# Kernel optimization log

Hardware: AMD Instinct MI355X
Metric: run time of the kernel (lower is better)

Reference implementation:

```python
import jax, jax.numpy as jnp
import numpy as np

N = 4096; D0 = 1024; D1 = 1280; H0 = 819; H1 = 1024; S = 819; K = 5


def setup_inputs() -> dict:
    key = jax.random.key(0)
    ks = jax.random.split(key, 20)
    def rn(k, shape, scale=1.0):
        return jax.random.normal(k, shape, dtype=jnp.float32) * scale
    inp = {}
    inp['x0'] = rn(ks[0], (N, D0))
    inp['x1'] = rn(ks[1], (N, D1))
    inp['we'] = jax.random.uniform(ks[2], (N, 2), dtype=jnp.float32, minval=0.1, maxval=1.0)
    # scale graphs ~1/100 so row-aggregated features stay in tanh's linear-ish range
    inp['g0'] = rn(ks[3], (N, N), 0.01)
    inp['g1'] = rn(ks[4], (N, N), 0.01)
    # Linear weights stored [in, out] (torch Linear applies x @ W.T + b); xavier-ish scale
    inp['We1_0'] = rn(ks[5], (D0, H0), D0 ** -0.5); inp['be1_0'] = jnp.zeros((H0,), jnp.float32)
    inp['We2_0'] = rn(ks[6], (H0, S), H0 ** -0.5);  inp['be2_0'] = jnp.zeros((S,), jnp.float32)
    inp['We1_1'] = rn(ks[7], (D1, H1), D1 ** -0.5); inp['be1_1'] = jnp.zeros((H1,), jnp.float32)
    inp['We2_1'] = rn(ks[8], (H1, S), H1 ** -0.5);  inp['be2_1'] = jnp.zeros((S,), jnp.float32)
    inp['Wd1_0'] = rn(ks[9], (S, H0), S ** -0.5);   inp['bd1_0'] = jnp.zeros((H0,), jnp.float32)
    inp['Wd2_0'] = rn(ks[10], (H0, D0), H0 ** -0.5); inp['bd2_0'] = jnp.zeros((D0,), jnp.float32)
    inp['Wd1_1'] = rn(ks[11], (S, H1), S ** -0.5);  inp['bd1_1'] = jnp.zeros((H1,), jnp.float32)
    inp['Wd2_1'] = rn(ks[12], (H1, D1), H1 ** -0.5); inp['bd2_1'] = jnp.zeros((D1,), jnp.float32)
    inp['Ww_0'] = rn(ks[13], (S, S), S ** -0.5)
    inp['Ww_1'] = rn(ks[14], (S, S), S ** -0.5)
    inp['Wf_0'] = rn(ks[15], (S, S), S ** -0.5)
    inp['Wf_1'] = rn(ks[16], (S, S), S ** -0.5)
    # stands in for the sklearn spectral-clustering centers (constant w.r.t. autodiff)
    inp['cluster_layer'] = rn(ks[17], (K, S), 0.1)
    return inp


def _gconv2(g, x, W1, b1, W2, b2):
    # tanh(Linear(g @ x)) twice: fusable gather-MLP chain
    h1 = jnp.tanh((g @ x) @ W1 + b1)
    return jnp.tanh((g @ h1) @ W2 + b2)


def reference(x0, x1, we, g0, g1,
              We1_0, be1_0, We2_0, be2_0, We1_1, be1_1, We2_1, be2_1,
              Wd1_0, bd1_0, Wd2_0, bd2_0, Wd1_1, bd1_1, Wd2_1, bd2_1,
              Ww_0, Ww_1, Wf_0, Wf_1, cluster_layer):
    # encoders
    h2_0 = _gconv2(g0, x0, We1_0, be1_0, We2_0, be2_0)  # [N, S]
    h2_1 = _gconv2(g1, x1, We1_1, be1_1, We2_1, be2_1)  # [N, S]
    # diag(we[:,i]) @ h_i  ==  broadcast row-scale (avoids O(N^2) diag matmul)
    weighted_sum = we[:, 0:1] * h2_0 + we[:, 1:2] * h2_1
    z = weighted_sum / jnp.sum(we, axis=1, keepdims=True)  # diag(1/sum) @ ws
    # inner-product adjacency decoders
    adj0 = jax.nn.sigmoid((z @ Ww_0) @ z.T)  # [N, N]
    adj1 = jax.nn.sigmoid((z @ Ww_1) @ z.T)
    # feature decoders with fusion weights
    rec0 = _gconv2(g0, jnp.tanh(z @ Wf_0), Wd1_0, bd1_0, Wd2_0, bd2_0)  # [N, D0]
    rec1 = _gconv2(g1, jnp.tanh(z @ Wf_1), Wd1_1, bd1_1, Wd2_1, bd2_1)  # [N, D1]
    # Student-t soft assignment to cluster centers
    d2 = jnp.sum((z[:, None, :] - cluster_layer[None, :, :]) ** 2, axis=2)  # [N, K]
    q = 1.0 / (1.0 + d2)
    q = q / jnp.sum(q, axis=1, keepdims=True)
    # target distribution p
    w = q ** 2 / jnp.sum(q, axis=0)
    p = w / jnp.sum(w, axis=1, keepdims=True)
    return (rec0, rec1, adj0, adj1, z, p, q, cluster_layer)
```

## Files before the change

### kernel.cpp

```cpp
#include <hip/hip_runtime.h>
#include <hip/hip_bf16.h>
#include <cstdint>
#include <cstddef>

typedef __bf16 bf16;
typedef __attribute__((ext_vector_type(8))) __bf16 bf16x8;
typedef __attribute__((ext_vector_type(4))) __bf16 bf16x4;
typedef __attribute__((ext_vector_type(4))) float f32x4;

__device__ __forceinline__ void gload_lds16(const void* g, void* l) {
  __builtin_amdgcn_global_load_lds(
      (const __attribute__((address_space(1))) uint32_t*)(uintptr_t)g,
      (__attribute__((address_space(3))) uint32_t*)(uintptr_t)l, 16, 0, 0);
}

struct GProb {
  const bf16* A; const bf16* Bt; const float* bias;
  float* Cf; bf16* Cb;
  int K, Npad, ldcf, ldcb, Ntrue, act;
};
struct GBatch { GProb p[4]; };

__global__ __launch_bounds__(256, 2)
void gemm_nt_batch(GBatch b)
{
  const GProb P = b.p[blockIdx.z];
  const long bn = (long)blockIdx.x * 128;
  if (bn >= P.Npad) return;

  __shared__ __align__(16) bf16 As[128 * 32];
  __shared__ __align__(16) bf16 Bs[128 * 32];

  const int K    = P.K;
  const int tid  = threadIdx.x;
  const int lane = tid & 63, wave = tid >> 6;
  const int wr = wave >> 1, wc = wave & 1;
  const int l15 = lane & 15, quad = lane >> 4;
  const long bm = (long)blockIdx.y * 128;

  long aoff[2], boff[2];
  int ldsoff[2];
#pragma unroll
  for (int s = 0; s < 2; ++s) {
    int slot = s * 256 + tid;
    int row = slot >> 2, cs = slot & 3;
    int gc = cs ^ (row & 3);
    aoff[s] = (bm + row) * (long)K + gc * 8;
    boff[s] = (bn + row) * (long)K + gc * 8;
    ldsoff[s] = (s * 256 + wave * 64) * 8;
  }

  const int cfr = (quad ^ (lane & 3)) * 8;
  int afr[4], bfr[4];
#pragma unroll
  for (int i = 0; i < 4; ++i) {
    afr[i] = (wr * 64 + i * 16 + l15) * 32 + cfr;
    bfr[i] = (wc * 64 + i * 16 + l15) * 32 + cfr;
  }

  f32x4 acc[4][4];
#pragma unroll
  for (int i = 0; i < 4; ++i)
#pragma unroll
    for (int j = 0; j < 4; ++j) acc[i][j] = {0.f, 0.f, 0.f, 0.f};

  for (int k0 = 0; k0 < K; k0 += 32) {
    __syncthreads();
    gload_lds16(P.A + aoff[0] + k0, As + ldsoff[0]);
    gload_lds16(P.A + aoff[1] + k0, As + ldsoff[1]);
    gload_lds16(P.Bt + boff[0] + k0, Bs + ldsoff[0]);
    gload_lds16(P.Bt + boff[1] + k0, Bs + ldsoff[1]);
    __syncthreads();

    bf16x8 av[4], bv[4];
#pragma unroll
    for (int i = 0; i < 4; ++i) av[i] = *(const bf16x8*)(As + afr[i]);
#pragma unroll
    for (int j = 0; j < 4; ++j) bv[j] = *(const bf16x8*)(Bs + bfr[j]);
#pragma unroll
    for (int i = 0; i < 4; ++i)
#pragma unroll
      for (int j = 0; j < 4; ++j)
        acc[i][j] = __builtin_amdgcn_mfma_f32_16x16x32_bf16(av[i], bv[j], acc[i][j], 0, 0, 0);
  }

  const long row0 = bm + wr * 64 + quad * 4;
  const long col0 = bn + wc * 64 + l15;
  const int act = P.act;
#pragma unroll
  for (int i = 0; i < 4; ++i) {
#pragma unroll
    for (int j = 0; j < 4; ++j) {
      long c = col0 + j * 16;
      float bb = P.bias ? P.bias[c] : 0.f;
#pragma unroll
      for (int t = 0; t < 4; ++t) {
        long r = row0 + i * 16 + t;
        float v = acc[i][j][t] + bb;
        if (act == 1) v = tanhf(v);
        else if (act == 2) v = 1.f / (1.f + __expf(-v));
        if (P.Cf && c < P.Ntrue) P.Cf[r * P.ldcf + c] = v;
        if (P.Cb) P.Cb[r * P.ldcb + c] = (bf16)v;
      }
    }
  }
}

struct TrBatch {
  const void* src[14]; bf16* dst[14];
  int R[14], C[14], Q[14], nbx[14], isb[14];
  int blkStart[15];
  int nprob;
};

__global__ void tr_batch(TrBatch a)
{
  __shared__ float tile[32][33];
  int pi = 0, b = blockIdx.x;
  while (b >= a.blkStart[pi + 1]) ++pi;
  const int rel = b - a.blkStart[pi];
  const int nbx = a.nbx[pi];
  const int q0 = (rel % nbx) * 32;
  const int p0 = (rel / nbx) * 32;
  const int R = a.R[pi], C = a.C[pi], Q = a.Q[pi];
  const bool isb = a.isb[pi] != 0;
  const void* src = a.src[pi];
  const int tx = threadIdx.x & 31, ty = threadIdx.x >> 5;
#pragma unroll
  for (int y = ty; y < 32; y += 8) {
    int r = q0 + y, c = p0 + tx;
    float v = 0.f;
    if (r < R && c < C)
      v = isb ? (float)((const bf16*)src)[(long)r * C + c]
              : ((const float*)src)[(long)r * C + c];
    tile[y][tx] = v;
  }
  __syncthreads();
  bf16* dst = a.dst[pi];
#pragma unroll
  for (int y = ty; y < 32; y += 8)
    dst[(long)(p0 + y) * Q + (q0 + tx)] = (bf16)tile[tx][y];
}

struct CvtB { const float* s[2]; bf16* d[2]; };
__global__ void cvt_batch(CvtB cb, long n)
{
  const float* s = cb.s[blockIdx.z];
  bf16* d = cb.d[blockIdx.z];
  long i = ((long)blockIdx.x * blockDim.x + threadIdx.x) * 4;
  if (i >= n) return;
  float4 v = *(const float4*)(s + i);
  bf16x4 o = {(bf16)v.x, (bf16)v.y, (bf16)v.z, (bf16)v.w};
  *(bf16x4*)(d + i) = o;
}

__global__ void zkern(const float* __restrict__ h20, const float* __restrict__ h21,
                      const float* __restrict__ we, float* __restrict__ zout,
                      bf16* __restrict__ zb)
{
  const int n = blockIdx.x;
  const float w0 = we[n * 2], w1 = we[n * 2 + 1];
  const float inv = 1.f / (w0 + w1);
  for (int c = threadIdx.x; c < 896; c += 256) {
    float v = (w0 * h20[(long)n * 896 + c] + w1 * h21[(long)n * 896 + c]) * inv;
    zb[(long)n * 896 + c] = (bf16)v;
    if (c < 819) zout[(long)n * 819 + c] = v;
  }
}

__global__ void qkern(const float* __restrict__ z, const float* __restrict__ cl,
                      float* __restrict__ qout)
{
  const int n = blockIdx.x;
  const int lane = threadIdx.x;
  float d0 = 0, d1 = 0, d2 = 0, d3 = 0, d4 = 0;
  for (int s = lane; s < 819; s += 64) {
    float zv = z[(long)n * 819 + s];
    float t0 = zv - cl[0 * 819 + s]; d0 += t0 * t0;
    float t1 = zv - cl[1 * 819 + s]; d1 += t1 * t1;
    float t2 = zv - cl[2 * 819 + s]; d2 += t2 * t2;
    float t3 = zv - cl[3 * 819 + s]; d3 += t3 * t3;
    float t4 = zv - cl[4 * 819 + s]; d4 += t4 * t4;
  }
#pragma unroll
  for (int off = 32; off > 0; off >>= 1) {
    d0 += __shfl_xor(d0, off);
    d1 += __shfl_xor(d1, off);
    d2 += __shfl_xor(d2, off);
    d3 += __shfl_xor(d3, off);
    d4 += __shfl_xor(d4, off);
  }
  if (lane == 0) {
    float q0 = 1.f / (1.f + d0), q1 = 1.f / (1.f + d1), q2 = 1.f / (1.f + d2);
    float q3 = 1.f / (1.f + d3), q4 = 1.f / (1.f + d4);
    float inv = 1.f / (q0 + q1 + q2 + q3 + q4);
    float* qr = qout + (long)n * 5;
    qr[0] = q0 * inv; qr[1] = q1 * inv; qr[2] = q2 * inv;
    qr[3] = q3 * inv; qr[4] = q4 * inv;
  }
}

__global__ void colsum_kern(const float* __restrict__ q, float* __restrict__ colsum)
{
  __shared__ float red[256];
  const int k = blockIdx.x;
  float s = 0.f;
  for (int n = threadIdx.x; n < 4096; n += 256) s += q[(long)n * 5 + k];
  red[threadIdx.x] = s;
  __syncthreads();
  for (int w = 128; w > 0; w >>= 1) {
    if (threadIdx.x < w) red[threadIdx.x] += red[threadIdx.x + w];
    __syncthreads();
  }
  if (threadIdx.x == 0) colsum[k] = red[0];
}

__global__ void pkern(const float* __restrict__ q, const float* __restrict__ colsum,
                      float* __restrict__ p)
{
  int n = blockIdx.x * blockDim.x + threadIdx.x;
  if (n >= 4096) return;
  float w[5], s = 0.f;
#pragma unroll
  for (int k = 0; k < 5; ++k) {
    float qv = q[(long)n * 5 + k];
    w[k] = qv * qv / colsum[k];
    s += w[k];
  }
  float inv = 1.f / s;
#pragma unroll
  for (int k = 0; k < 5; ++k) p[(long)n * 5 + k] = w[k] * inv;
}

struct BiasArgs {
  const float* src[8];
  float* dst[8];
  int n[8];
  int np[8];
};

__global__ void biaspad(BiasArgs a)
{
  int b = blockIdx.x;
  for (int i = threadIdx.x; i < a.np[b]; i += blockDim.x)
    a.dst[b][i] = (i < a.n[b]) ? a.src[b][i] : 0.f;
}

extern "C" void kernel_launch(void* const* d_in, const int* in_sizes, int n_in,
                              void* d_out, int out_size, void* d_ws, size_t ws_size,
                              hipStream_t stream)
{
  (void)in_sizes; (void)n_in; (void)out_size; (void)ws_size;
  const float* x0    = (const float*)d_in[0];
  const float* x1    = (const float*)d_in[1];
  const float* we    = (const float*)d_in[2];
  const float* g0    = (const float*)d_in[3];
  const float* g1    = (const float*)d_in[4];
  const float* We1_0 = (const float*)d_in[5];
  const float* be1_0 = (const float*)d_in[6];
  const float* We2_0 = (const float*)d_in[7];
  const float* be2_0 = (const float*)d_in[8];
  const float* We1_1 = (const float*)d_in[9];
  const float* be1_1 = (const float*)d_in[10];
  const float* We2_1 = (const float*)d_in[11];
  const float* be2_1 = (const float*)d_in[12];
  const float* Wd1_0 = (const float*)d_in[13];
  const float* bd1_0 = (const float*)d_in[14];
  const float* Wd2_0 = (const float*)d_in[15];
  const float* bd2_0 = (const float*)d_in[16];
  const float* Wd1_1 = (const float*)d_in[17];
  const float* bd1_1 = (const float*)d_in[18];
  const float* Wd2_1 = (const float*)d_in[19];
  const float* bd2_1 = (const float*)d_in[20];
  const float* Ww0   = (const float*)d_in[21];
  const float* Ww1   = (const float*)d_in[22];
  const float* Wf0   = (const float*)d_in[23];
  const float* Wf1   = (const float*)d_in[24];
  const float* clus  = (const float*)d_in[25];
  float* out = (float*)d_out;

  const size_t OFF_REC0 = 0;
  const size_t OFF_REC1 = 4194304;
  const size_t OFF_ADJ0 = 9437184;
  const size_t OFF_ADJ1 = 26214400;
  const size_t OFF_Z    = 42991616;
  const size_t OFF_P    = 46346240;
  const size_t OFF_Q    = 46366720;
  const size_t OFF_CL   = 46387200;

  char* ws = (char*)d_ws;
  size_t off = 0;
  auto alloc = [&](size_t bytes) -> void* {
    off = (off + 255) & ~(size_t)255;
    void* p = ws + off;
    off += bytes;
    return p;
  };
  const long N = 4096;
  bf16* g0b   = (bf16*)alloc((size_t)N * 4096 * 2);
  bf16* g1b   = (bf16*)alloc((size_t)N * 4096 * 2);
  bf16* BTe10 = (bf16*)alloc((size_t)896 * 1024 * 2);
  bf16* BTe20 = (bf16*)alloc((size_t)896 * 896 * 2);
  bf16* BTe11 = (bf16*)alloc((size_t)1024 * 1280 * 2);
  bf16* BTe21 = (bf16*)alloc((size_t)896 * 1024 * 2);
  bf16* BTd10 = (bf16*)alloc((size_t)896 * 896 * 2);
  bf16* BTd20 = (bf16*)alloc((size_t)1024 * 896 * 2);
  bf16* BTd11 = (bf16*)alloc((size_t)1024 * 896 * 2);
  bf16* BTd21 = (bf16*)alloc((size_t)1280 * 1024 * 2);
  bf16* BTw0  = (bf16*)alloc((size_t)896 * 896 * 2);
  bf16* BTw1  = (bf16*)alloc((size_t)896 * 896 * 2);
  bf16* BTf0  = (bf16*)alloc((size_t)896 * 896 * 2);
  bf16* BTf1  = (bf16*)alloc((size_t)896 * 896 * 2);
  float* pbe10 = (float*)alloc(896 * 4);
  float* pbe20 = (float*)alloc(896 * 4);
  float* pbe11 = (float*)alloc(1024 * 4);
  float* pbe21 = (float*)alloc(896 * 4);
  float* pbd10 = (float*)alloc(896 * 4);
  float* pbd20 = (float*)alloc(1024 * 4);
  float* pbd11 = (float*)alloc(1024 * 4);
  float* pbd21 = (float*)alloc(1280 * 4);
  float* h20f  = (float*)alloc((size_t)N * 896 * 4);
  float* h21f  = (float*)alloc((size_t)N * 896 * 4);
  bf16* zb     = (bf16*)alloc((size_t)N * 896 * 2);
  float* colsum = (float*)alloc(64);
  bf16* xT0 = (bf16*)alloc((size_t)1024 * 4096 * 2);
  bf16* xT1 = (bf16*)alloc((size_t)1280 * 4096 * 2);
  bf16* u0  = (bf16*)alloc((size_t)N * 1024 * 2);
  bf16* u1  = (bf16*)alloc((size_t)N * 1280 * 2);
  bf16* h0  = (bf16*)alloc((size_t)N * 896 * 2);
  bf16* h1b = (bf16*)alloc((size_t)N * 1024 * 2);
  bf16* y0  = (bf16*)alloc((size_t)N * 896 * 2);
  bf16* y1  = (bf16*)alloc((size_t)N * 896 * 2);
  bf16* t0b = (bf16*)alloc((size_t)N * 896 * 2);
  bf16* t1b = (bf16*)alloc((size_t)N * 896 * 2);

  {
    CvtB cb;
    cb.s[0] = g0; cb.d[0] = g0b;
    cb.s[1] = g1; cb.d[1] = g1b;
    cvt_batch<<<dim3(16384, 1, 2), 256, 0, stream>>>(cb, N * 4096);
  }

  {
    TrBatch tb{};
    tb.nprob = 0; tb.blkStart[0] = 0;
    auto addTr = [&](const void* s, bf16* d, int R, int C, int P, int Q, int isb) {
      int i = tb.nprob++;
      tb.src[i] = s; tb.dst[i] = d;
      tb.R[i] = R; tb.C[i] = C; tb.Q[i] = Q; tb.isb[i] = isb;
      tb.nbx[i] = Q / 32;
      tb.blkStart[i + 1] = tb.blkStart[i] + (Q / 32) * (P / 32);
    };
    addTr(x0, xT0, 4096, 1024, 1024, 4096, 0);
    addTr(x1, xT1, 4096, 1280, 1280, 4096, 0);
    addTr(We1_0, BTe10, 1024, 819, 896, 1024, 0);
    addTr(We2_0, BTe20, 819, 819, 896, 896, 0);
    addTr(We1_1, BTe11, 1280, 1024, 1024, 1280, 0);
    addTr(We2_1, BTe21, 1024, 819, 896, 1024, 0);
    addTr(Wd1_0, BTd10, 819, 819, 896, 896, 0);
    addTr(Wd2_0, BTd20, 819, 1024, 1024, 896, 0);
    addTr(Wd1_1, BTd11, 819, 1024, 1024, 896, 0);
    addTr(Wd2_1, BTd21, 1024, 1280, 1280, 1024, 0);
    addTr(Ww0, BTw0, 819, 819, 896, 896, 0);
    addTr(Ww1, BTw1, 819, 819, 896, 896, 0);
    addTr(Wf0, BTf0, 819, 819, 896, 896, 0);
    addTr(Wf1, BTf1, 819, 819, 896, 896, 0);
    tr_batch<<<tb.blkStart[tb.nprob], 256, 0, stream>>>(tb);
  }

  BiasArgs ba;
  {
    const float* bsrc[8] = {be1_0, be2_0, be1_1, be2_1, bd1_0, bd2_0, bd1_1, bd2_1};
    float* bdst[8] = {pbe10, pbe20, pbe11, pbe21, pbd10, pbd20, pbd11, pbd21};
    int bn_[8] = {819, 819, 1024, 819, 819, 1024, 1024, 1280};
    int bnp[8] = {896, 896, 1024, 896, 896, 1024, 1024, 1280};
    for (int i = 0; i < 8; ++i) { ba.src[i] = bsrc[i]; ba.dst[i] = bdst[i]; ba.n[i] = bn_[i]; ba.np[i] = bnp[i]; }
  }
  biaspad<<<8, 256, 0, stream>>>(ba);

  GBatch gb{};
  int np = 0, maxN = 0;
  auto beg = [&]() { np = 0; maxN = 0; };
  auto add = [&](const bf16* A, const bf16* Bt, const float* bias,
                 float* Cf, int ldcf, bf16* Cb, int ldcb,
                 int K, int Npad, int Ntrue, int act) {
    gb.p[np].A = A; gb.p[np].Bt = Bt; gb.p[np].bias = bias;
    gb.p[np].Cf = Cf; gb.p[np].Cb = Cb;
    gb.p[np].K = K; gb.p[np].Npad = Npad;
    gb.p[np].ldcf = ldcf; gb.p[np].ldcb = ldcb;
    gb.p[np].Ntrue = Ntrue; gb.p[np].act = act;
    ++np;
    if (Npad > maxN) maxN = Npad;
  };
  auto go = [&]() {
    gemm_nt_batch<<<dim3(maxN / 128, 32, np), 256, 0, stream>>>(gb);
  };
  auto trb2 = [&](const bf16* s0, int C0, const bf16* s1, int C1) {
    TrBatch tb{};
    tb.nprob = 2; tb.blkStart[0] = 0;
    tb.src[0] = s0; tb.dst[0] = xT0; tb.R[0] = 4096; tb.C[0] = C0; tb.Q[0] = 4096;
    tb.isb[0] = 1; tb.nbx[0] = 128; tb.blkStart[1] = 128 * (C0 / 32);
    tb.src[1] = s1; tb.dst[1] = xT1; tb.R[1] = 4096; tb.C[1] = C1; tb.Q[1] = 4096;
    tb.isb[1] = 1; tb.nbx[1] = 128; tb.blkStart[2] = tb.blkStart[1] + 128 * (C1 / 32);
    tr_batch<<<tb.blkStart[2], 256, 0, stream>>>(tb);
  };

  beg();
  add(g0b, xT0, nullptr, nullptr, 0, u0, 1024, 4096, 1024, 1024, 0);
  add(g1b, xT1, nullptr, nullptr, 0, u1, 1280, 4096, 1280, 1280, 0);
  go();
  beg();
  add(u0, BTe10, pbe10, nullptr, 0, h0, 896, 1024, 896, 896, 1);
  add(u1, BTe11, pbe11, nullptr, 0, h1b, 1024, 1280, 1024, 1024, 1);
  go();
  trb2(h0, 896, h1b, 1024);
  beg();
  add(g0b, xT0, nullptr, nullptr, 0, h0, 896, 4096, 896, 896, 0);
  add(g1b, xT1, nullptr, nullptr, 0, h1b, 1024, 4096, 1024, 1024, 0);
  go();
  beg();
  add(h0, BTe20, pbe20, h20f, 896, nullptr, 0, 896, 896, 896, 1);
  add(h1b, BTe21, pbe21, h21f, 896, nullptr, 0, 1024, 896, 896, 1);
  go();

  zkern<<<4096, 256, 0, stream>>>(h20f, h21f, we, out + OFF_Z, zb);

  beg();
  add(zb, BTw0, nullptr, nullptr, 0, y0, 896, 896, 896, 896, 0);
  add(zb, BTw1, nullptr, nullptr, 0, y1, 896, 896, 896, 896, 0);
  add(zb, BTf0, nullptr, nullptr, 0, t0b, 896, 896, 896, 896, 1);
  add(zb, BTf1, nullptr, nullptr, 0, t1b, 896, 896, 896, 896, 1);
  go();
  beg();
  add(y0, zb, nullptr, out + OFF_ADJ0, 4096, nullptr, 0, 896, 4096, 4096, 2);
  add(y1, zb, nullptr, out + OFF_ADJ1, 4096, nullptr, 0, 896, 4096, 4096, 2);
  go();

  trb2(t0b, 896, t1b, 896);
  beg();
  add(g0b, xT0, nullptr, nullptr, 0, u0, 896, 4096, 896, 896, 0);
  add(g1b, xT1, nullptr, nullptr, 0, u1, 896, 4096, 896, 896, 0);
  go();
  beg();
  add(u0, BTd10, pbd10, nullptr, 0, h0, 896, 896, 896, 896, 1);
  add(u1, BTd11, pbd11, nullptr, 0, h1b, 1024, 896, 1024, 1024, 1);
  go();
  trb2(h0, 896, h1b, 1024);
  beg();
  add(g0b, xT0, nullptr, nullptr, 0, u0, 896, 4096, 896, 896, 0);
  add(g1b, xT1, nullptr, nullptr, 0, u1, 1024, 4096, 1024, 1024, 0);
  go();
  beg();
  add(u0, BTd20, pbd20, out + OFF_REC0, 1024, nullptr, 0, 896, 1024, 1024, 1);
  add(u1, BTd21, pbd21, out + OFF_REC1, 1280, nullptr, 0, 1024, 1280, 1280, 1);
  go();

  qkern<<<4096, 64, 0, stream>>>(out + OFF_Z, clus, out + OFF_Q);
  colsum_kern<<<5, 256, 0, stream>>>(out + OFF_Q, colsum);
  pkern<<<16, 256, 0, stream>>>(out + OFF_Q, colsum, out + OFF_P);
  hipMemcpyAsync(out + OFF_CL, (const void*)clus, 4095 * sizeof(float),
                 hipMemcpyDeviceToDevice, stream);
}
```

Before: 1.234 ms.

## Add double-buffered GEMM variant for small grids and batch adjacency with decoder gathers

```diff
diff --git a/kernel.cpp b/kernel.cpp
--- a/kernel.cpp
+++ b/kernel.cpp
@@ -21,6 +21,27 @@
 };
 struct GBatch { GProb p[4]; };
 
+#define STAGE_(Ad, Bd, kk) do {                                   \
+    gload_lds16(P.A + aoff[0] + (kk), (Ad) + ldsoff[0]);          \
+    gload_lds16(P.A + aoff[1] + (kk), (Ad) + ldsoff[1]);          \
+    gload_lds16(P.Bt + boff[0] + (kk), (Bd) + ldsoff[0]);         \
+    gload_lds16(P.Bt + boff[1] + (kk), (Bd) + ldsoff[1]);         \
+  } while (0)
+
+#define COMPUTE_(Ab, Bb) do {                                     \
+    bf16x8 av[4], bv[4];                                          \
+    _Pragma("unroll")                                             \
+    for (int i_ = 0; i_ < 4; ++i_) av[i_] = *(const bf16x8*)((Ab) + afr[i_]); \
+    _Pragma("unroll")                                             \
+    for (int j_ = 0; j_ < 4; ++j_) bv[j_] = *(const bf16x8*)((Bb) + bfr[j_]); \
+    _Pragma("unroll")                                             \
+    for (int i_ = 0; i_ < 4; ++i_)                                \
+      _Pragma("unroll")                                           \
+      for (int j_ = 0; j_ < 4; ++j_)                              \
+        acc[i_][j_] = __builtin_amdgcn_mfma_f32_16x16x32_bf16(av[i_], bv[j_], acc[i_][j_], 0, 0, 0); \
+  } while (0)
+
+template<int PIPE>
 __global__ __launch_bounds__(256, 2)
 void gemm_nt_batch(GBatch b)
 {
@@ -28,8 +49,8 @@
   const long bn = (long)blockIdx.x * 128;
   if (bn >= P.Npad) return;
 
-  __shared__ __align__(16) bf16 As[128 * 32];
-  __shared__ __align__(16) bf16 Bs[128 * 32];
+  __shared__ __align__(16) bf16 As0[128 * 32];
+  __shared__ __align__(16) bf16 Bs0[128 * 32];
 
   const int K    = P.K;
   const int tid  = threadIdx.x;
@@ -64,24 +85,38 @@
 #pragma unroll
     for (int j = 0; j < 4; ++j) acc[i][j] = {0.f, 0.f, 0.f, 0.f};
 
-  for (int k0 = 0; k0 < K; k0 += 32) {
-    __syncthreads();
-    gload_lds16(P.A + aoff[0] + k0, As + ldsoff[0]);
-    gload_lds16(P.A + aoff[1] + k0, As + ldsoff[1]);
-    gload_lds16(P.Bt + boff[0] + k0, Bs + ldsoff[0]);
-    gload_lds16(P.Bt + boff[1] + k0, Bs + ldsoff[1]);
-    __syncthreads();
-
-    bf16x8 av[4], bv[4];
-#pragma unroll
-    for (int i = 0; i < 4; ++i) av[i] = *(const bf16x8*)(As + afr[i]);
-#pragma unroll
-    for (int j = 0; j < 4; ++j) bv[j] = *(const bf16x8*)(Bs + bfr[j]);
-#pragma unroll
-    for (int i = 0; i < 4; ++i)
-#pragma unroll
-      for (int j = 0; j < 4; ++j)
-        acc[i][j] = __builtin_amdgcn_mfma_f32_16x16x32_bf16(av[i], bv[j], acc[i][j], 0, 0, 0);
+  if constexpr (PIPE == 0) {
+    for (int k0 = 0; k0 < K; k0 += 32) {
+      __syncthreads();
+      STAGE_(As0, Bs0, k0);
+      __syncthreads();
+      COMPUTE_(As0, Bs0);
+    }
+  } else {
+    __shared__ __align__(16) bf16 As1[128 * 32];
+    __shared__ __align__(16) bf16 Bs1[128 * 32];
+    const int nt = K >> 5;
+    STAGE_(As0, Bs0, 0);
+    for (int t = 0; t < nt; t += 2) {
+      STAGE_(As1, Bs1, (t + 1) * 32);
+      asm volatile("s_waitcnt vmcnt(4)" ::: "memory");
+      __builtin_amdgcn_s_barrier();
+      __builtin_amdgcn_sched_barrier(0);
+      COMPUTE_(As0, Bs0);
+      asm volatile("s_waitcnt lgkmcnt(0)" ::: "memory");
+      __builtin_amdgcn_s_barrier();
+      if (t + 2 < nt) {
+        STAGE_(As0, Bs0, (t + 2) * 32);
+        asm volatile("s_waitcnt vmcnt(4)" ::: "memory");
+      } else {
+        asm volatile("s_waitcnt vmcnt(0)" ::: "memory");
+      }
+      __builtin_amdgcn_s_barrier();
+      __builtin_amdgcn_sched_barrier(0);
+      COMPUTE_(As1, Bs1);
+      asm volatile("s_waitcnt lgkmcnt(0)" ::: "memory");
+      __builtin_amdgcn_s_barrier();
+    }
   }
 
   const long row0 = bm + wr * 64 + quad * 4;
@@ -393,7 +428,13 @@
     if (Npad > maxN) maxN = Npad;
   };
   auto go = [&]() {
-    gemm_nt_batch<<<dim3(maxN / 128, 32, np), 256, 0, stream>>>(gb);
+    int active = 0;
+    for (int i = 0; i < np; ++i) active += gb.p[i].Npad / 128;
+    dim3 grid(maxN / 128, 32, np);
+    if (active * 32 < 768)
+      gemm_nt_batch<1><<<grid, 256, 0, stream>>>(gb);
+    else
+      gemm_nt_batch<0><<<grid, 256, 0, stream>>>(gb);
   };
   auto trb2 = [&](const bf16* s0, int C0, const bf16* s1, int C1) {
     TrBatch tb{};
@@ -431,16 +472,15 @@
   add(zb, BTf0, nullptr, nullptr, 0, t0b, 896, 896, 896, 896, 1);
   add(zb, BTf1, nullptr, nullptr, 0, t1b, 896, 896, 896, 896, 1);
   go();
-  beg();
+
+  trb2(t0b, 896, t1b, 896);
+  beg();
+  add(g0b, xT0, nullptr, nullptr, 0, u0, 896, 4096, 896, 896, 0);
+  add(g1b, xT1, nullptr, nullptr, 0, u1, 896, 4096, 896, 896, 0);
   add(y0, zb, nullptr, out + OFF_ADJ0, 4096, nullptr, 0, 896, 4096, 4096, 2);
   add(y1, zb, nullptr, out + OFF_ADJ1, 4096, nullptr, 0, 896, 4096, 4096, 2);
   go();
 
-  trb2(t0b, 896, t1b, 896);
-  beg();
-  add(g0b, xT0, nullptr, nullptr, 0, u0, 896, 4096, 896, 896, 0);
-  add(g1b, xT1, nullptr, nullptr, 0, u1, 896, 4096, 896, 896, 0);
-  go();
   beg();
   add(u0, BTd10, pbd10, nullptr, 0, h0, 896, 896, 896, 896, 1);
   add(u1, BTd11, pbd11, nullptr, 0, h1b, 1024, 896, 1024, 1024, 1);
```

Measured after the change: 1.317 ms. 1.07x slower.

## Reassociate encoder graph convs, split-K graph GEMMs, and strengthen LDS swizzle

Applied to the files above, without the earlier changes.

```diff
diff --git a/kernel.cpp b/kernel.cpp
--- a/kernel.cpp
+++ b/kernel.cpp
@@ -16,15 +16,18 @@
 
 struct GProb {
   const bf16* A; const bf16* Bt; const float* bias;
-  float* Cf; bf16* Cb;
+  float* Cf; bf16* Cb; float* Cp;
   int K, Npad, ldcf, ldcb, Ntrue, act;
 };
 struct GBatch { GProb p[4]; };
 
+template<int SPLIT>
 __global__ __launch_bounds__(256, 2)
 void gemm_nt_batch(GBatch b)
 {
-  const GProb P = b.p[blockIdx.z];
+  const int prob = (SPLIT == 2) ? ((int)blockIdx.z >> 1) : (int)blockIdx.z;
+  const int kz   = (SPLIT == 2) ? ((int)blockIdx.z & 1) : 0;
+  const GProb P = b.p[prob];
   const long bn = (long)blockIdx.x * 128;
   if (bn >= P.Npad) return;
 
@@ -44,13 +47,13 @@
   for (int s = 0; s < 2; ++s) {
     int slot = s * 256 + tid;
     int row = slot >> 2, cs = slot & 3;
-    int gc = cs ^ (row & 3);
+    int gc = (cs ^ (row & 3) ^ ((row >> 2) & 3)) & 3;
     aoff[s] = (bm + row) * (long)K + gc * 8;
     boff[s] = (bn + row) * (long)K + gc * 8;
     ldsoff[s] = (s * 256 + wave * 64) * 8;
   }
 
-  const int cfr = (quad ^ (lane & 3)) * 8;
+  const int cfr = ((quad ^ (lane & 3) ^ ((lane >> 2) & 3)) & 3) * 8;
   int afr[4], bfr[4];
 #pragma unroll
   for (int i = 0; i < 4; ++i) {
@@ -64,7 +67,9 @@
 #pragma unroll
     for (int j = 0; j < 4; ++j) acc[i][j] = {0.f, 0.f, 0.f, 0.f};
 
-  for (int k0 = 0; k0 < K; k0 += 32) {
+  const int Kseg = K / SPLIT;
+  const int kbeg = kz * Kseg;
+  for (int k0 = kbeg; k0 < kbeg + Kseg; k0 += 32) {
     __syncthreads();
     gload_lds16(P.A + aoff[0] + k0, As + ldsoff[0]);
     gload_lds16(P.A + aoff[1] + k0, As + ldsoff[1]);
@@ -86,23 +91,70 @@
 
   const long row0 = bm + wr * 64 + quad * 4;
   const long col0 = bn + wc * 64 + l15;
-  const int act = P.act;
-#pragma unroll
-  for (int i = 0; i < 4; ++i) {
-#pragma unroll
-    for (int j = 0; j < 4; ++j) {
-      long c = col0 + j * 16;
-      float bb = P.bias ? P.bias[c] : 0.f;
-#pragma unroll
-      for (int t = 0; t < 4; ++t) {
-        long r = row0 + i * 16 + t;
-        float v = acc[i][j][t] + bb;
-        if (act == 1) v = tanhf(v);
-        else if (act == 2) v = 1.f / (1.f + __expf(-v));
-        if (P.Cf && c < P.Ntrue) P.Cf[r * P.ldcf + c] = v;
-        if (P.Cb) P.Cb[r * P.ldcb + c] = (bf16)v;
+  if constexpr (SPLIT == 2) {
+    float* Cp = P.Cp + (long)kz * 4096 * P.Npad;
+#pragma unroll
+    for (int i = 0; i < 4; ++i)
+#pragma unroll
+      for (int j = 0; j < 4; ++j)
+#pragma unroll
+        for (int t = 0; t < 4; ++t)
+          Cp[(row0 + i * 16 + t) * (long)P.Npad + col0 + j * 16] = acc[i][j][t];
+  } else {
+    const int act = P.act;
+#pragma unroll
+    for (int i = 0; i < 4; ++i) {
+#pragma unroll
+      for (int j = 0; j < 4; ++j) {
+        long c = col0 + j * 16;
+        float bb = P.bias ? P.bias[c] : 0.f;
+#pragma unroll
+        for (int t = 0; t < 4; ++t) {
+          long r = row0 + i * 16 + t;
+          float v = acc[i][j][t] + bb;
+          if (act == 1) v = tanhf(v);
+          else if (act == 2) v = 1.f / (1.f + __expf(-v));
+          if (P.Cf && c < P.Ntrue) P.Cf[r * P.ldcf + c] = v;
+          if (P.Cb) P.Cb[r * P.ldcb + c] = (bf16)v;
+        }
       }
     }
+  }
+}
+
+struct CProb {
+  const float* part; const float* bias;
+  float* Cf; bf16* Cb;
+  int Npad, ldcf, ldcb, Ntrue, act;
+};
+struct CBatch { CProb p[2]; };
+
+__global__ void combine_batch(CBatch cb)
+{
+  const CProb P = cb.p[blockIdx.z];
+  const int row = blockIdx.x;
+  const int c4 = threadIdx.x * 4;
+  if (c4 >= P.Npad) return;
+  const long base = (long)row * P.Npad + c4;
+  float4 a = *(const float4*)(P.part + base);
+  float4 b = *(const float4*)(P.part + (long)4096 * P.Npad + base);
+  float v[4] = {a.x + b.x, a.y + b.y, a.z + b.z, a.w + b.w};
+  if (P.bias) {
+    float4 bi = *(const float4*)(P.bias + c4);
+    v[0] += bi.x; v[1] += bi.y; v[2] += bi.z; v[3] += bi.w;
+  }
+#pragma unroll
+  for (int t = 0; t < 4; ++t) {
+    if (P.act == 1) v[t] = tanhf(v[t]);
+    else if (P.act == 2) v[t] = 1.f / (1.f + __expf(-v[t]));
+  }
+  if (P.Cf && c4 < P.Ntrue) {
+    float* o = P.Cf + (long)row * P.ldcf + c4;
+    o[0] = v[0]; o[1] = v[1]; o[2] = v[2]; o[3] = v[3];
+  }
+  if (P.Cb) {
+    bf16x4 o = {(bf16)v[0], (bf16)v[1], (bf16)v[2], (bf16)v[3]};
+    *(bf16x4*)(P.Cb + (long)row * P.ldcb + c4) = o;
   }
 }
 
@@ -142,13 +194,13 @@
     dst[(long)(p0 + y) * Q + (q0 + tx)] = (bf16)tile[tx][y];
 }
 
-struct CvtB { const float* s[2]; bf16* d[2]; };
-__global__ void cvt_batch(CvtB cb, long n)
+struct CvtB { const float* s[4]; bf16* d[4]; long n[4]; };
+__global__ void cvt_batch(CvtB cb)
 {
   const float* s = cb.s[blockIdx.z];
   bf16* d = cb.d[blockIdx.z];
   long i = ((long)blockIdx.x * blockDim.x + threadIdx.x) * 4;
-  if (i >= n) return;
+  if (i >= cb.n[blockIdx.z]) return;
   float4 v = *(const float4*)(s + i);
   bf16x4 o = {(bf16)v.x, (bf16)v.y, (bf16)v.z, (bf16)v.w};
   *(bf16x4*)(d + i) = o;
@@ -299,6 +351,8 @@
   const long N = 4096;
   bf16* g0b   = (bf16*)alloc((size_t)N * 4096 * 2);
   bf16* g1b   = (bf16*)alloc((size_t)N * 4096 * 2);
+  bf16* x0b   = (bf16*)alloc((size_t)N * 1024 * 2);
+  bf16* x1b   = (bf16*)alloc((size_t)N * 1280 * 2);
   bf16* BTe10 = (bf16*)alloc((size_t)896 * 1024 * 2);
   bf16* BTe20 = (bf16*)alloc((size_t)896 * 896 * 2);
   bf16* BTe11 = (bf16*)alloc((size_t)1024 * 1280 * 2);
@@ -333,12 +387,16 @@
   bf16* y1  = (bf16*)alloc((size_t)N * 896 * 2);
   bf16* t0b = (bf16*)alloc((size_t)N * 896 * 2);
   bf16* t1b = (bf16*)alloc((size_t)N * 896 * 2);
+  float* partA = (float*)alloc((size_t)2 * N * 1024 * 4);
+  float* partB = (float*)alloc((size_t)2 * N * 1024 * 4);
 
   {
     CvtB cb;
-    cb.s[0] = g0; cb.d[0] = g0b;
-    cb.s[1] = g1; cb.d[1] = g1b;
-    cvt_batch<<<dim3(16384, 1, 2), 256, 0, stream>>>(cb, N * 4096);
+    cb.s[0] = g0; cb.d[0] = g0b; cb.n[0] = N * 4096;
+    cb.s[1] = g1; cb.d[1] = g1b; cb.n[1] = N * 4096;
+    cb.s[2] = x0; cb.d[2] = x0b; cb.n[2] = N * 1024;
+    cb.s[3] = x1; cb.d[3] = x1b; cb.n[3] = N * 1280;
+    cvt_batch<<<dim3(16384, 1, 4), 256, 0, stream>>>(cb);
   }
 
   {
@@ -351,8 +409,6 @@
       tb.nbx[i] = Q / 32;
       tb.blkStart[i + 1] = tb.blkStart[i] + (Q / 32) * (P / 32);
     };
-    addTr(x0, xT0, 4096, 1024, 1024, 4096, 0);
-    addTr(x1, xT1, 4096, 1280, 1280, 4096, 0);
     addTr(We1_0, BTe10, 1024, 819, 896, 1024, 0);
     addTr(We2_0, BTe20, 819, 819, 896, 896, 0);
     addTr(We1_1, BTe11, 1280, 1024, 1024, 1280, 0);
@@ -380,20 +436,34 @@
 
   GBatch gb{};
   int np = 0, maxN = 0;
-  auto beg = [&]() { np = 0; maxN = 0; };
+  auto beg = [&]() { np = 0; maxN = 0; gb = GBatch{}; };
   auto add = [&](const bf16* A, const bf16* Bt, const float* bias,
                  float* Cf, int ldcf, bf16* Cb, int ldcb,
                  int K, int Npad, int Ntrue, int act) {
     gb.p[np].A = A; gb.p[np].Bt = Bt; gb.p[np].bias = bias;
-    gb.p[np].Cf = Cf; gb.p[np].Cb = Cb;
+    gb.p[np].Cf = Cf; gb.p[np].Cb = Cb; gb.p[np].Cp = nullptr;
     gb.p[np].K = K; gb.p[np].Npad = Npad;
     gb.p[np].ldcf = ldcf; gb.p[np].ldcb = ldcb;
     gb.p[np].Ntrue = Ntrue; gb.p[np].act = act;
     ++np;
     if (Npad > maxN) maxN = Npad;
   };
-  auto go = [&]() {
-    gemm_nt_batch<<<dim3(maxN / 128, 32, np), 256, 0, stream>>>(gb);
+  auto addS = [&](const bf16* A, const bf16* Bt, float* Cp, int K, int Npad) {
+    gb.p[np].A = A; gb.p[np].Bt = Bt; gb.p[np].bias = nullptr;
+    gb.p[np].Cf = nullptr; gb.p[np].Cb = nullptr; gb.p[np].Cp = Cp;
+    gb.p[np].K = K; gb.p[np].Npad = Npad;
+    gb.p[np].ldcf = 0; gb.p[np].ldcb = 0; gb.p[np].Ntrue = 0; gb.p[np].act = 0;
+    ++np;
+    if (Npad > maxN) maxN = Npad;
+  };
+  auto goN = [&]() { gemm_nt_batch<1><<<dim3(maxN / 128, 32, np), 256, 0, stream>>>(gb); };
+  auto goS = [&]() { gemm_nt_batch<2><<<dim3(maxN / 128, 32, np * 2), 256, 0, stream>>>(gb); };
+  auto comb = [&](const float* bias0, float* Cf0, int ldf0, int Nt0, bf16* Cb0, int ldb0, int Np0, int act0,
+                  const float* bias1, float* Cf1, int ldf1, int Nt1, bf16* Cb1, int ldb1, int Np1, int act1) {
+    CBatch cb;
+    cb.p[0] = {partA, bias0, Cf0, Cb0, Np0, ldf0, ldb0, Nt0, act0};
+    cb.p[1] = {partB, bias1, Cf1, Cb1, Np1, ldf1, ldb1, Nt1, act1};
+    combine_batch<<<dim3(4096, 1, 2), 256, 0, stream>>>(cb);
   };
   auto trb2 = [&](const bf16* s0, int C0, const bf16* s1, int C1) {
     TrBatch tb{};
@@ -406,22 +476,27 @@
   };
 
   beg();
-  add(g0b, xT0, nullptr, nullptr, 0, u0, 1024, 4096, 1024, 1024, 0);
-  add(g1b, xT1, nullptr, nullptr, 0, u1, 1280, 4096, 1280, 1280, 0);
-  go();
-  beg();
-  add(u0, BTe10, pbe10, nullptr, 0, h0, 896, 1024, 896, 896, 1);
-  add(u1, BTe11, pbe11, nullptr, 0, h1b, 1024, 1280, 1024, 1024, 1);
-  go();
-  trb2(h0, 896, h1b, 1024);
-  beg();
-  add(g0b, xT0, nullptr, nullptr, 0, h0, 896, 4096, 896, 896, 0);
-  add(g1b, xT1, nullptr, nullptr, 0, h1b, 1024, 4096, 1024, 1024, 0);
-  go();
-  beg();
-  add(h0, BTe20, pbe20, h20f, 896, nullptr, 0, 896, 896, 896, 1);
-  add(h1b, BTe21, pbe21, h21f, 896, nullptr, 0, 1024, 896, 896, 1);
-  go();
+  add(x0b, BTe10, nullptr, nullptr, 0, u0, 896, 1024, 896, 896, 0);
+  add(x1b, BTe11, nullptr, nullptr, 0, u1, 1024, 1280, 1024, 1024, 0);
+  goN();
+  trb2(u0, 896, u1, 1024);
+  beg();
+  addS(g0b, xT0, partA, 4096, 896);
+  addS(g1b, xT1, partB, 4096, 1024);
+  goS();
+  comb(pbe10, nullptr, 0, 0, h0, 896, 896, 1,
+       pbe11, nullptr, 0, 0, h1b, 1024, 1024, 1);
+  beg();
+  add(h0, BTe20, nullptr, nullptr, 0, u0, 896, 896, 896, 896, 0);
+  add(h1b, BTe21, nullptr, nullptr, 0, u1, 896, 1024, 896, 896, 0);
+  goN();
+  trb2(u0, 896, u1, 896);
+  beg();
+  addS(g0b, xT0, partA, 4096, 896);
+  addS(g1b, xT1, partB, 4096, 896);
+  goS();
+  comb(pbe20, h20f, 896, 896, nullptr, 0, 896, 1,
+       pbe21, h21f, 896, 896, nullptr, 0, 896, 1);
 
   zkern<<<4096, 256, 0, stream>>>(h20f, h21f, we, out + OFF_Z, zb);
 
@@ -430,30 +505,34 @@
   add(zb, BTw1, nullptr, nullptr, 0, y1, 896, 896, 896, 896, 0);
   add(zb, BTf0, nullptr, nullptr, 0, t0b, 896, 896, 896, 896, 1);
   add(zb, BTf1, nullptr, nullptr, 0, t1b, 896, 896, 896, 896, 1);
-  go();
+  goN();
   beg();
   add(y0, zb, nullptr, out + OFF_ADJ0, 4096, nullptr, 0, 896, 4096, 4096, 2);
   add(y1, zb, nullptr, out + OFF_ADJ1, 4096, nullptr, 0, 896, 4096, 4096, 2);
-  go();
+  goN();
 
   trb2(t0b, 896, t1b, 896);
   beg();
-  add(g0b, xT0, nullptr, nullptr, 0, u0, 896, 4096, 896, 896, 0);
-  add(g1b, xT1, nullptr, nullptr, 0, u1, 896, 4096, 896, 896, 0);
-  go();
+  addS(g0b, xT0, partA, 4096, 896);
+  addS(g1b, xT1, partB, 4096, 896);
+  goS();
+  comb(nullptr, nullptr, 0, 0, u0, 896, 896, 0,
+       nullptr, nullptr, 0, 0, u1, 896, 896, 0);
   beg();
   add(u0, BTd10, pbd10, nullptr, 0, h0, 896, 896, 896, 896, 1);
   add(u1, BTd11, pbd11, nullptr, 0, h1b, 1024, 896, 1024, 1024, 1);
-  go();
+  goN();
   trb2(h0, 896, h1b, 1024);
   beg();
-  add(g0b, xT0, nullptr, nullptr, 0, u0, 896, 4096, 896, 896, 0);
-  add(g1b, xT1, nullptr, nullptr, 0, u1, 1024, 4096, 1024, 1024, 0);
-  go();
+  addS(g0b, xT0, partA, 4096, 896);
+  addS(g1b, xT1, partB, 4096, 1024);
+  goS();
+  comb(nullptr, nullptr, 0, 0, u0, 896, 896, 0,
+       nullptr, nullptr, 0, 0, u1, 1024, 1024, 0);
   beg();
   add(u0, BTd20, pbd20, out + OFF_REC0, 1024, nullptr, 0, 896, 1024, 1024, 1);
   add(u1, BTd21, pbd21, out + OFF_REC1, 1280, nullptr, 0, 1024, 1280, 1280, 1);
-  go();
+  goN();
 
   qkern<<<4096, 64, 0, stream>>>(out + OFF_Z, clus, out + OFF_Q);
   colsum_kern<<<5, 256, 0, stream>>>(out + OFF_Q, colsum);
```

Result: slower. 1.272 ms (+3.1%).
